# Optimization experiments

Hardware: AMD Instinct MI355X
Metric: run time of the kernel (lower is better)

The kernel has to match this reference:

```python
import jax, jax.numpy as jnp
import numpy as np

N_QUBITS = 10
DEPTH = 5
NUM_CLASSES = 2
DIM = 2 ** N_QUBITS  # 1024


def _rx(t):
    # RX(t) = [[cos(t/2), -i sin(t/2)], [-i sin(t/2), cos(t/2)]]
    c, s = jnp.cos(t / 2), jnp.sin(t / 2)
    zr = jnp.zeros_like(t)
    a = jax.lax.complex(c, zr)
    b = jax.lax.complex(zr, -s)
    return jnp.stack([jnp.stack([a, b]), jnp.stack([b, a])]).astype(jnp.complex64)


def _rz(t):
    # RZ(t) = diag(e^{-it/2}, e^{it/2})
    c, s = jnp.cos(t / 2), jnp.sin(t / 2)
    e = jax.lax.complex(c, -s)
    z = jnp.zeros_like(e)
    return jnp.stack([jnp.stack([e, z]), jnp.stack([z, jnp.conj(e)])]).astype(jnp.complex64)


def _apply_1q(state, U, wire):
    # state: (B, 2, ..., 2); wire axis is wire+1 (wire 0 = most significant bit)
    s = jnp.moveaxis(state, wire + 1, -1)
    s = s @ U.T
    return jnp.moveaxis(s, -1, wire + 1)


def _apply_c1q(state, U, ctrl, tgt):
    # controlled-U: apply U on tgt where ctrl qubit is |1>
    s = jnp.moveaxis(state, ctrl + 1, 1)  # (B, 2_ctrl, rest...)
    ax = tgt + 1 if tgt < ctrl else tgt   # tgt axis inside s[:, k]
    s1 = s[:, 1]
    s1 = jnp.moveaxis(s1, ax, -1) @ U.T
    s1 = jnp.moveaxis(s1, -1, ax)
    s = jnp.stack([s[:, 0], s1], axis=1)
    return jnp.moveaxis(s, 1, ctrl + 1)


def _circuit(x, weights, weights_1, weights_2):
    B = x.shape[0]
    x = x.reshape(B, -1)
    x = jnp.pad(x, ((0, 0), (0, DIM - x.shape[1])))  # pad_with=0
    x = x / jnp.linalg.norm(x, axis=1, keepdims=True)  # normalize=True
    state = jax.lax.complex(x, jnp.zeros_like(x)).reshape((B,) + (2,) * N_QUBITS)
    for d in range(DEPTH):
        for i in range(N_QUBITS):
            state = _apply_1q(state, _rx(weights[d, i, 0]), i)
            state = _apply_1q(state, _rz(weights[d, i, 1]), i)
            state = _apply_1q(state, _rx(weights[d, i, 2]), i)
        r = 1 if d % 2 == 0 else 3  # alternating entangler range (CCQC)
        for i in range(N_QUBITS):
            c = (i + r) % N_QUBITS
            state = _apply_c1q(state, _rz(weights[d, i, 3]), c, i)
            state = _apply_c1q(state, _rx(weights[d, i, 4]), c, i)
        state = _apply_1q(state, _rx(weights_1[d]), 0)
        state = _apply_1q(state, _rz(weights_2[d]), 0)
    probs = (jnp.abs(state) ** 2).reshape(B, DIM)
    # <Z_w> signs: bit w (MSB-first) of each basis index
    bits = (jnp.arange(DIM)[None, :] >> (N_QUBITS - 1 - jnp.arange(N_QUBITS)[:, None])) & 1
    zsign = (1 - 2 * bits).astype(probs.dtype)  # (n_qubits, DIM)
    return probs @ zsign.T  # (B, n_qubits)


def setup_inputs() -> dict:
    key = jax.random.key(0)
    ks = jax.random.split(key, 5)
    B = 8192
    x = jax.random.normal(ks[0], (B, 784), dtype=jnp.float32)
    y = jax.random.randint(ks[1], (B,), 0, NUM_CLASSES)
    weights = jax.random.uniform(ks[2], (DEPTH, N_QUBITS, 5), jnp.float32, 0.0, 2 * np.pi)
    weights_1 = jax.random.uniform(ks[3], (DEPTH,), jnp.float32, 0.0, 2 * np.pi)
    weights_2 = jax.random.uniform(ks[4], (DEPTH,), jnp.float32, 0.0, 2 * np.pi)
    return {"x": x, "y": y, "weights": weights, "weights_1": weights_1, "weights_2": weights_2}


def reference(x, y, weights, weights_1, weights_2):
    expz = _circuit(x, weights, weights_1, weights_2)
    logits = expz[:, :NUM_CLASSES]
    logp = jax.nn.log_softmax(logits, axis=-1)
    nll = -jnp.take_along_axis(logp, y[:, None].astype(jnp.int32), axis=1)[:, 0]
    return jnp.mean(nll)  # CrossEntropyLoss (mean reduction)
```

## Files before the change

kernel.cpp:

```cpp
#include <hip/hip_runtime.h>


namespace {

typedef float f32x2 __attribute__((ext_vector_type(2)));
typedef __fp16 fp16x2 __attribute__((ext_vector_type(2)));
typedef _Float16 f16x8 __attribute__((ext_vector_type(8)));
typedef float f32x4v __attribute__((ext_vector_type(4)));

__device__ __forceinline__ f32x2 pk_mul(f32x2 a, f32x2 b) {
  f32x2 d;
  asm("v_pk_mul_f32 %0, %1, %2" : "=v"(d) : "v"(a), "v"(b));
  return d;
}
__device__ __forceinline__ f32x2 pk_fma(f32x2 a, f32x2 b, f32x2 c) {
  f32x2 d;
  asm("v_pk_fma_f32 %0, %1, %2, %3" : "=v"(d) : "v"(a), "v"(b), "v"(c));
  return d;
}
__device__ __forceinline__ f32x2 pk_fma_swap1(f32x2 a, f32x2 b, f32x2 c) {
  f32x2 d;
  asm("v_pk_fma_f32 %0, %1, %2, %3 op_sel:[0,1,0] op_sel_hi:[1,0,1]"
      : "=v"(d) : "v"(a), "v"(b), "v"(c));
  return d;
}
__device__ __forceinline__ f32x2 cmulp(f32x2 cr2, f32x2 ci2, f32x2 v) {
  return pk_fma_swap1(ci2, v, pk_mul(cr2, v));
}
__device__ __forceinline__ f32x2 cmad(f32x2 acc, f32x2 cr2, f32x2 ci2, f32x2 v) {
  return pk_fma_swap1(ci2, v, pk_fma(cr2, v, acc));
}

__device__ __forceinline__ f32x2 shfl_xor2(f32x2 v, int lm) {
  f32x2 r;
  r.x = __shfl_xor(v.x, lm, 64);
  r.y = __shfl_xor(v.y, lm, 64);
  return r;
}
template <int CTRL>
__device__ __forceinline__ f32x2 dpp_xor2(f32x2 v) {
  f32x2 r;
  const int ix = __builtin_bit_cast(int, v.x);
  const int iy = __builtin_bit_cast(int, v.y);
  r.x = __builtin_bit_cast(float,
      __builtin_amdgcn_update_dpp(0, ix, CTRL, 0xF, 0xF, true));
  r.y = __builtin_bit_cast(float,
      __builtin_amdgcn_update_dpp(0, iy, CTRL, 0xF, 0xF, true));
  return r;
}
__device__ __forceinline__ f32x2 shfl_fast(f32x2 v, const int lm) {
  if (lm == 1) return dpp_xor2<0xB1>(v);
  if (lm == 2) return dpp_xor2<0x4E>(v);
  return shfl_xor2(v, lm);
}
__device__ __forceinline__ f32x2 sel2(bool c, f32x2 a, f32x2 b) {
  f32x2 r; r.x = c ? a.x : b.x; r.y = c ? a.y : b.y; return r;
}

struct c2 { float r, i; };
struct m2c { c2 a00, a01, a10, a11; };

__device__ __forceinline__ c2 cmul(c2 x, c2 y) { return {x.r*y.r - x.i*y.i, x.r*y.i + x.i*y.r}; }
__device__ __forceinline__ c2 cadd(c2 x, c2 y) { return {x.r + y.r, x.i + y.i}; }
__device__ __forceinline__ c2 conjc(c2 a) { return {a.r, -a.i}; }
__device__ __forceinline__ m2c mmul(m2c A, m2c B) {
  m2c C;
  C.a00 = cadd(cmul(A.a00, B.a00), cmul(A.a01, B.a10));
  C.a01 = cadd(cmul(A.a00, B.a01), cmul(A.a01, B.a11));
  C.a10 = cadd(cmul(A.a10, B.a00), cmul(A.a11, B.a10));
  C.a11 = cadd(cmul(A.a10, B.a01), cmul(A.a11, B.a11));
  return C;
}
__device__ __forceinline__ m2c mrx(float t) {
  float c = cosf(0.5f * t), s = sinf(0.5f * t);
  return { {c, 0.f}, {0.f, -s}, {0.f, -s}, {c, 0.f} };
}
__device__ __forceinline__ m2c mrz(float t) {
  float c = cosf(0.5f * t), s = sinf(0.5f * t);
  return { {c, -s}, {0.f, 0.f}, {0.f, 0.f}, {c, s} };
}

__global__ void make_prog(const float* __restrict__ w, const float* __restrict__ w1,
                          const float* __restrict__ w2, float* __restrict__ prog) {
  const int t = threadIdx.x;
  m2c U{}; int slot = -1;
  if (t < 50) {
    const int d = t / 10, i = t % 10;
    const float* p = w + (d * 10 + i) * 5;
    U = mmul(mrx(p[2]), mmul(mrz(p[1]), mrx(p[0])));
    if (i == 0 && d > 0) {
      m2c U0 = mmul(mrz(w2[d - 1]), mrx(w1[d - 1]));
      U = mmul(U, U0);
    }
    const int dd = 4 - d;
    const int base = (dd == 0) ? 0 : 21 + (dd - 1) * 20;
    slot = base + ((d == 4) ? 11 : 10) + (9 - i);
  } else if (t < 100) {
    const int s = t - 50; const int d = s / 10, i = s % 10;
    const float* p = w + (d * 10 + i) * 5;
    U = mmul(mrx(p[4]), mrz(p[3]));
    const int dd = 4 - d;
    const int base = (dd == 0) ? 0 : 21 + (dd - 1) * 20;
    slot = base + ((d == 4) ? 1 : 0) + (9 - i);
  } else if (t == 100) {
    U = mmul(mrz(w2[4]), mrx(w1[4]));
    slot = 0;
  }
  if (slot >= 0) {
    const c2 A[4] = {conjc(U.a00), conjc(U.a10), conjc(U.a01), conjc(U.a11)};
    float* o = prog + slot * 16;
    #pragma unroll
    for (int q = 0; q < 4; ++q) {
      o[q*4 + 0] = A[q].r; o[q*4 + 1] = A[q].r;
      o[q*4 + 2] = -A[q].i; o[q*4 + 3] = A[q].i;
    }
  }
}

struct MatP { f32x2 u00r, u00i, u01r, u01i, u10r, u10i, u11r, u11i; };

__device__ __forceinline__ MatP ldmatG(const float* __restrict__ prog, int slot) {
  const float4* p = reinterpret_cast<const float4*>(prog + slot * 16);
  float4 a = p[0], b = p[1], c = p[2], d = p[3];
  MatP m;
  m.u00r = f32x2{a.x, a.y}; m.u00i = f32x2{a.z, a.w};
  m.u01r = f32x2{b.x, b.y}; m.u01i = f32x2{b.z, b.w};
  m.u10r = f32x2{c.x, c.y}; m.u10i = f32x2{c.z, c.w};
  m.u11r = f32x2{d.x, d.y}; m.u11i = f32x2{d.z, d.w};
  return m;
}

__device__ __forceinline__ void g_xlane(f32x2 (&s)[4], const int lm,
                                        const f32x2 cAr, const f32x2 cAi,
                                        const f32x2 cBr, const f32x2 cBi,
                                        const int cm_reg) {
  #pragma unroll
  for (int k = 0; k < 4; ++k) {
    if (cm_reg && !(k & cm_reg)) continue;
    const f32x2 p = shfl_fast(s[k], lm);
    s[k] = cmad(cmulp(cAr, cAi, s[k]), cBr, cBi, p);
  }
}
__device__ __forceinline__ void g_local(f32x2 (&s)[4], const int kb, const MatP m,
                                        const int cm_reg) {
  const int tm = 1 << kb;
  #pragma unroll
  for (int k0 = 0; k0 < 4; ++k0) {
    if (k0 & tm) continue;
    if (cm_reg && !(k0 & cm_reg)) continue;
    const int k1 = k0 | tm;
    const f32x2 a = s[k0], b = s[k1];
    s[k0] = cmad(cmulp(m.u00r, m.u00i, a), m.u01r, m.u01i, b);
    s[k1] = cmad(cmulp(m.u10r, m.u10i, a), m.u11r, m.u11i, b);
  }
}
__device__ __forceinline__ void g_xwave(f32x2 (&s)[4], f32x2* lxb, const int wv,
                                        const int lane, const int tb,
                                        const f32x2 cAr, const f32x2 cAi,
                                        const f32x2 cBr, const f32x2 cBi,
                                        const int cm_reg) {
  #pragma unroll
  for (int k = 0; k < 4; ++k) lxb[(wv * 4 + k) * 64 + lane] = s[k];
  __syncthreads();
  const int pw = wv ^ (1 << tb);
  #pragma unroll
  for (int k = 0; k < 4; ++k) {
    if (cm_reg && !(k & cm_reg)) continue;
    const f32x2 p = lxb[(pw * 4 + k) * 64 + lane];
    s[k] = cmad(cmulp(cAr, cAi, s[k]), cBr, cBi, p);
  }
}

__device__ __forceinline__ void apply_gate(f32x2 (&s)[4], f32x2* lxb, const int wv,
                                           const int lane, const MatP mIn,
                                           const int bt, const int bc) {
  MatP m = mIn;
  const f32x2 oner{1.f, 1.f}, zero{0.f, 0.f};
  int cm_reg = 0;
  bool fold = false, cl = true;
  if (bc >= 8)      { cl = ((wv >> (bc - 8)) & 1) != 0; fold = true; }
  else if (bc >= 6) { cm_reg = 1 << (bc - 6); }
  else if (bc >= 0) { cl = ((lane >> bc) & 1) != 0; fold = true; }

  if (bt >= 8) {
    const int tb = bt - 8;
    const bool hi = ((wv >> tb) & 1) != 0;
    f32x2 cAr = sel2(hi, m.u11r, m.u00r), cAi = sel2(hi, m.u11i, m.u00i);
    f32x2 cBr = sel2(hi, m.u10r, m.u01r), cBi = sel2(hi, m.u10i, m.u01i);
    if (fold) {
      cAr = sel2(cl, cAr, oner); cAi = sel2(cl, cAi, zero);
      cBr = sel2(cl, cBr, zero); cBi = sel2(cl, cBi, zero);
    }
    g_xwave(s, lxb, wv, lane, tb, cAr, cAi, cBr, cBi, cm_reg);
  } else if (bt >= 6) {
    if (fold) {
      m.u00r = sel2(cl, m.u00r, oner); m.u00i = sel2(cl, m.u00i, zero);
      m.u01r = sel2(cl, m.u01r, zero); m.u01i = sel2(cl, m.u01i, zero);
      m.u10r = sel2(cl, m.u10r, zero); m.u10i = sel2(cl, m.u10i, zero);
      m.u11r = sel2(cl, m.u11r, oner); m.u11i = sel2(cl, m.u11i, zero);
    }
    g_local(s, bt - 6, m, cm_reg);
  } else {
    const bool hi = ((lane >> bt) & 1) != 0;
    f32x2 cAr = sel2(hi, m.u11r, m.u00r), cAi = sel2(hi, m.u11i, m.u00i);
    f32x2 cBr = sel2(hi, m.u10r, m.u01r), cBi = sel2(hi, m.u10i, m.u01i);
    if (fold) {
      cAr = sel2(cl, cAr, oner); cAi = sel2(cl, cAi, zero);
      cBr = sel2(cl, cBr, zero); cBi = sel2(cl, cBi, zero);
    }
    g_xlane(s, 1 << bt, cAr, cAi, cBr, cBi, cm_reg);
  }
}

__global__ __launch_bounds__(256) void qprep(const float* __restrict__ prog,
                                             const float* __restrict__ x,
                                             _Float16* __restrict__ Wt,
                                             _Float16* __restrict__ Xh) {
  const int tid = threadIdx.x;
  if (blockIdx.x >= 1024) {
    const int t = (blockIdx.x - 1024) * 256 + tid;
    const int b = t >> 7;
    const int j = (t & 127) * 8;
    if (j >= 832) return;
    union { fp16x2 h2[4]; f16x8 h8; } u;
    if (j < 784) {
      const float4* p = reinterpret_cast<const float4*>(x + (size_t)b * 784 + j);
      const float4 v0 = p[0], v1 = p[1];
      u.h2[0] = __builtin_amdgcn_cvt_pkrtz(v0.x, v0.y);
      u.h2[1] = __builtin_amdgcn_cvt_pkrtz(v0.z, v0.w);
      u.h2[2] = __builtin_amdgcn_cvt_pkrtz(v1.x, v1.y);
      u.h2[3] = __builtin_amdgcn_cvt_pkrtz(v1.z, v1.w);
    } else {
      #pragma unroll
      for (int q = 0; q < 4; ++q) u.h2[q] = __builtin_amdgcn_cvt_pkrtz(0.f, 0.f);
    }
    *reinterpret_cast<f16x8*>(Xh + (size_t)b * 1024 + j) = u.h8;
    return;
  }

  __shared__ f32x2 lx[2][1024];

  const int lane = tid & 63;
  const int wv = tid >> 6;
  const int n = blockIdx.x;

  f32x2 s[4];
  #pragma unroll
  for (int k = 0; k < 4; ++k) {
    const int j = (wv << 8) | (k << 6) | lane;
    s[k].x = (j == n) ? 1.f : 0.f;
    s[k].y = 0.f;
  }

  int p = 0, ph = 0;
  #pragma unroll
  for (int dd = 0; dd < 5; ++dd) {
    const int d = 4 - dd;
    if (d == 4) {
      apply_gate(s, &lx[ph & 1][0], wv, lane, ldmatG(prog, p), 9, -1);
      ++p; ++ph;
    }
    const int r = (d & 1) ? 3 : 1;
    #pragma unroll
    for (int ii = 0; ii < 10; ++ii) {
      const int i = 9 - ii;
      const int c = (i + r) % 10;
      const int bt = 9 - i, bc = 9 - c;
      apply_gate(s, &lx[ph & 1][0], wv, lane, ldmatG(prog, p), bt, bc);
      ++p; if (bt >= 8) ++ph;
    }
    #pragma unroll
    for (int ii = 0; ii < 10; ++ii) {
      const int i = 9 - ii;
      const int bt = 9 - i;
      apply_gate(s, &lx[ph & 1][0], wv, lane, ldmatG(prog, p), bt, -1);
      ++p; if (bt >= 8) ++ph;
    }
  }

  #pragma unroll
  for (int k = 0; k < 4; ++k) {
    const int j = (wv << 8) | (k << 6) | lane;
    Wt[(size_t)(2 * n) * 1024 + j] = (_Float16)s[k].x;
    Wt[(size_t)(2 * n + 1) * 1024 + j] = (_Float16)(-s[k].y);
  }
}

#define GZ_NSTEP 13

__device__ __forceinline__ void stage_tiles(const _Float16* __restrict__ gA,
                                            const _Float16* __restrict__ gB,
                                            _Float16* sA, _Float16* sB,
                                            int k0, int wv, int lane) {
  const int rIn = lane >> 3;
  const int colh = ((lane & 7) ^ rIn) * 8;
  #pragma unroll
  for (int c = 0; c < 2; ++c) {
    const int chunk = wv * 2 + c;
    const size_t grow = (size_t)(chunk * 8 + rIn) * 1024 + k0 + colh;
    auto* la = (__attribute__((address_space(3))) void*)(sA + chunk * 512 + lane * 8);
    __builtin_amdgcn_global_load_lds(
        (const __attribute__((address_space(1))) void*)(gA + grow), la, 16, 0, 0);
    auto* lb = (__attribute__((address_space(3))) void*)(sB + chunk * 512 + lane * 8);
    __builtin_amdgcn_global_load_lds(
        (const __attribute__((address_space(1))) void*)(gB + grow), lb, 16, 0, 0);
  }
}

__device__ __forceinline__ int lds_off(int row, int slot) {
  return row * 64 + ((slot ^ (row & 7)) * 8);
}

__global__ __launch_bounds__(512) void gemm_z(const _Float16* __restrict__ Xh,
                                              const _Float16* __restrict__ Wt,
                                              float* __restrict__ part, int B) {
  __shared__ _Float16 smA[2][128 * 64];
  __shared__ _Float16 smB[2][128 * 64];

  const int tid = threadIdx.x;
  const int lane = tid & 63;
  const int wv = tid >> 6;
  const int wm = wv >> 1;
  const int wn = wv & 1;
  const int row0 = blockIdx.x * 128;
  const int n0 = blockIdx.y * 128;

  const _Float16* gA = Xh + (size_t)row0 * 1024;
  const _Float16* gB = Wt + (size_t)n0 * 1024;

  const int lr = lane & 15;
  const int lq = lane >> 4;

  f32x4v acc[2][4];
  #pragma unroll
  for (int m = 0; m < 2; ++m)
    #pragma unroll
    for (int f = 0; f < 4; ++f) acc[m][f] = f32x4v{0.f, 0.f, 0.f, 0.f};

  stage_tiles(gA, gB, smA[0], smB[0], 0, wv, lane);
  __syncthreads();

  for (int t = 0; t < GZ_NSTEP; ++t) {
    const int cur = t & 1;
    if (t + 1 < GZ_NSTEP)
      stage_tiles(gA, gB, smA[cur ^ 1], smB[cur ^ 1], (t + 1) * 64, wv, lane);

    #pragma unroll
    for (int kk = 0; kk < 2; ++kk) {
      const int slot = kk * 4 + lq;
      f16x8 a[2], b[4];
      #pragma unroll
      for (int m = 0; m < 2; ++m) {
        const int row = wm * 32 + m * 16 + lr;
        a[m] = *reinterpret_cast<const f16x8*>(&smA[cur][lds_off(row, slot)]);
      }
      #pragma unroll
      for (int f = 0; f < 4; ++f) {
        const int row = wn * 64 + f * 16 + lr;
        b[f] = *reinterpret_cast<const f16x8*>(&smB[cur][lds_off(row, slot)]);
      }
      #pragma unroll
      for (int m = 0; m < 2; ++m)
        #pragma unroll
        for (int f = 0; f < 4; ++f)
          acc[m][f] = __builtin_amdgcn_mfma_f32_16x16x32_f16(a[m], b[f], acc[m][f], 0, 0, 0);
    }
    __syncthreads();
  }

  const int pp = blockIdx.y * 2 + wn;
  #pragma unroll
  for (int m = 0; m < 2; ++m) {
    f32x4v p = f32x4v{0.f, 0.f, 0.f, 0.f};
    #pragma unroll
    for (int f = 0; f < 4; ++f) p += acc[m][f] * acc[m][f];
    #pragma unroll
    for (int msk = 1; msk < 16; msk <<= 1) {
      p.x += __shfl_xor(p.x, msk, 64);
      p.y += __shfl_xor(p.y, msk, 64);
      p.z += __shfl_xor(p.z, msk, 64);
      p.w += __shfl_xor(p.w, msk, 64);
    }
    if (lr == 0) {
      const int rbase = row0 + wm * 32 + m * 16 + lq * 4;
      float* dst = part + (size_t)pp * B + rbase;
      dst[0] = p.x; dst[1] = p.y; dst[2] = p.z; dst[3] = p.w;
    }
  }
}

__global__ __launch_bounds__(256) void nll_part(const float* __restrict__ part,
                                                const int* __restrict__ y,
                                                float* __restrict__ out2, int B) {
  const int row = blockIdx.x * 256 + threadIdx.x;
  float q0 = 0.f, q1 = 0.f, nn = 0.f;
  #pragma unroll
  for (int pp = 0; pp < 32; ++pp) {
    const float P = part[(size_t)pp * B + row];
    q0 += (pp & 16) ? -P : P;
    q1 += (pp & 8) ? -P : P;
    nn += P;
  }
  const float z0 = q0 / nn, z1 = q1 / nn;
  const float mx = fmaxf(z0, z1);
  const float lse = mx + logf(expf(z0 - mx) + expf(z1 - mx));
  const float ly = (y[row] == 0) ? z0 : z1;
  float s = lse - ly;
  #pragma unroll
  for (int msk = 1; msk < 64; msk <<= 1) s += __shfl_xor(s, msk, 64);
  __shared__ float red[4];
  if ((threadIdx.x & 63) == 0) red[threadIdx.x >> 6] = s;
  __syncthreads();
  if (threadIdx.x == 0) out2[blockIdx.x] = red[0] + red[1] + red[2] + red[3];
}

__global__ void nll_final(const float* __restrict__ out2, float* __restrict__ out,
                          int nblk, float scale) {
  const int t = threadIdx.x;
  float s = (t < nblk) ? out2[t] : 0.f;
  #pragma unroll
  for (int msk = 1; msk < 64; msk <<= 1) s += __shfl_xor(s, msk, 64);
  if (t == 0) out[0] = s * scale;
}

}

extern "C" void kernel_launch(void* const* d_in, const int* in_sizes, int n_in,
                              void* d_out, int out_size, void* d_ws, size_t ws_size,
                              hipStream_t stream) {
  const float* x  = (const float*)d_in[0];
  const int*   y  = (const int*)d_in[1];
  const float* w  = (const float*)d_in[2];
  const float* w1 = (const float*)d_in[3];
  const float* w2 = (const float*)d_in[4];
  float* out = (float*)d_out;

  const int B = in_sizes[0] / 784;

  char* ws = (char*)d_ws;
  _Float16* Wt   = (_Float16*)ws;
  _Float16* Xh   = (_Float16*)(ws + (size_t)2048 * 1024 * 2);
  float*    part = (float*)(ws + (size_t)2048 * 1024 * 2 + (size_t)B * 1024 * 2);
  float*    out2 = part + (size_t)32 * B;
  float*    prog = out2 + 64;

  make_prog<<<1, 128, 0, stream>>>(w, w1, w2, prog);
  qprep<<<1024 + (B * 128) / 256, 256, 0, stream>>>(prog, x, Wt, Xh);
  gemm_z<<<dim3(B / 128, 16), 512, 0, stream>>>(Xh, Wt, part, B);
  nll_part<<<B / 256, 256, 0, stream>>>(part, y, out2, B);
  nll_final<<<1, 64, 0, stream>>>(out2, out, B / 256, 1.0f / (float)B);
}
```

Measured before the change: 89.05 us.

## Fuse single-qubit rotation gates into following controlled gates in prep kernel

Folds each single-qubit U1 gate into the next controlled gate on the same target when no intervening gate touches that qubit. The controlled gate then applies V1 on the control=0 branch and VC*V1 on the control=1 branch, which cuts the number of gate passes, shuffles and LDS barriers in the unitary-building qprep kernel. The program layout doubles to two matrices per slot, and the fused path adds select overhead. This affects only the small Wt-generation stage, not the main GEMM.

```diff
diff --git a/kernel.cpp b/kernel.cpp
--- a/kernel.cpp
+++ b/kernel.cpp
@@ -71,6 +71,9 @@
   C.a11 = cadd(cmul(A.a10, B.a01), cmul(A.a11, B.a11));
   return C;
 }
+__device__ __forceinline__ m2c madj(m2c U) {
+  return { conjc(U.a00), conjc(U.a10), conjc(U.a01), conjc(U.a11) };
+}
 __device__ __forceinline__ m2c mrx(float t) {
   float c = cosf(0.5f * t), s = sinf(0.5f * t);
   return { {c, 0.f}, {0.f, -s}, {0.f, -s}, {c, 0.f} };
@@ -80,47 +83,78 @@
   return { {c, -s}, {0.f, 0.f}, {0.f, 0.f}, {c, s} };
 }
 
+__device__ __forceinline__ bool fusable(int d, int i) {
+  return (d & 1) ? (i >= 3) : (i >= 1);
+}
+
 __global__ void make_prog(const float* __restrict__ w, const float* __restrict__ w1,
                           const float* __restrict__ w2, float* __restrict__ prog) {
   const int t = threadIdx.x;
-  m2c U{}; int slot = -1;
-  if (t < 50) {
-    const int d = t / 10, i = t % 10;
-    const float* p = w + (d * 10 + i) * 5;
-    U = mmul(mrx(p[2]), mmul(mrz(p[1]), mrx(p[0])));
+  int kind = -1, od = 0, oi = 0, p = 0;
+  for (int dd = 0; dd < 5; ++dd) {
+    const int d = 4 - dd;
+    if (d == 4) { if (p == t) kind = 0; ++p; }
+    for (int ii = 0; ii < 10; ++ii) {
+      const int i = 9 - ii;
+      if (p == t) { kind = (d <= 3 && fusable(d, i)) ? 2 : 1; od = d; oi = i; }
+      ++p;
+    }
+    for (int ii = 0; ii < 10; ++ii) {
+      const int i = 9 - ii;
+      if (d >= 1 && fusable(d - 1, i)) continue;
+      if (p == t) { kind = 3; od = d; oi = i; }
+      ++p;
+    }
+  }
+  if (kind < 0) return;
+
+  auto u1mat = [&](int d, int i) -> m2c {
+    const float* pw = w + (d * 10 + i) * 5;
+    m2c U = mmul(mrx(pw[2]), mmul(mrz(pw[1]), mrx(pw[0])));
     if (i == 0 && d > 0) {
       m2c U0 = mmul(mrz(w2[d - 1]), mrx(w1[d - 1]));
       U = mmul(U, U0);
     }
-    const int dd = 4 - d;
-    const int base = (dd == 0) ? 0 : 21 + (dd - 1) * 20;
-    slot = base + ((d == 4) ? 11 : 10) + (9 - i);
-  } else if (t < 100) {
-    const int s = t - 50; const int d = s / 10, i = s % 10;
-    const float* p = w + (d * 10 + i) * 5;
-    U = mmul(mrx(p[4]), mrz(p[3]));
-    const int dd = 4 - d;
-    const int base = (dd == 0) ? 0 : 21 + (dd - 1) * 20;
-    slot = base + ((d == 4) ? 1 : 0) + (9 - i);
-  } else if (t == 100) {
-    U = mmul(mrz(w2[4]), mrx(w1[4]));
-    slot = 0;
-  }
-  if (slot >= 0) {
-    const c2 A[4] = {conjc(U.a00), conjc(U.a10), conjc(U.a01), conjc(U.a11)};
-    float* o = prog + slot * 16;
-    #pragma unroll
-    for (int q = 0; q < 4; ++q) {
-      o[q*4 + 0] = A[q].r; o[q*4 + 1] = A[q].r;
-      o[q*4 + 2] = -A[q].i; o[q*4 + 3] = A[q].i;
-    }
+    return U;
+  };
+  auto cumat = [&](int d, int i) -> m2c {
+    const float* pw = w + (d * 10 + i) * 5;
+    return mmul(mrx(pw[4]), mrz(pw[3]));
+  };
+
+  m2c A0{}, A1{};
+  if (kind == 0) {
+    A0 = madj(mmul(mrz(w2[4]), mrx(w1[4])));
+    A1 = A0;
+  } else if (kind == 1) {
+    A0 = madj(cumat(od, oi));
+    A1 = A0;
+  } else if (kind == 2) {
+    m2c V1 = madj(u1mat(od + 1, oi));
+    m2c VC = madj(cumat(od, oi));
+    A0 = V1;
+    A1 = mmul(VC, V1);
+  } else {
+    A0 = madj(u1mat(od, oi));
+    A1 = A0;
+  }
+
+  float* o = prog + t * 32;
+  const c2 e0[4] = {A0.a00, A0.a01, A0.a10, A0.a11};
+  const c2 e1[4] = {A1.a00, A1.a01, A1.a10, A1.a11};
+  #pragma unroll
+  for (int q = 0; q < 4; ++q) {
+    o[q*4 + 0] = e0[q].r; o[q*4 + 1] = e0[q].r;
+    o[q*4 + 2] = -e0[q].i; o[q*4 + 3] = e0[q].i;
+    o[16 + q*4 + 0] = e1[q].r; o[16 + q*4 + 1] = e1[q].r;
+    o[16 + q*4 + 2] = -e1[q].i; o[16 + q*4 + 3] = e1[q].i;
   }
 }
 
 struct MatP { f32x2 u00r, u00i, u01r, u01i, u10r, u10i, u11r, u11i; };
 
-__device__ __forceinline__ MatP ldmatG(const float* __restrict__ prog, int slot) {
-  const float4* p = reinterpret_cast<const float4*>(prog + slot * 16);
+__device__ __forceinline__ MatP ldmatG2(const float* __restrict__ prog, int slot, int half) {
+  const float4* p = reinterpret_cast<const float4*>(prog + slot * 32 + half * 16);
   float4 a = p[0], b = p[1], c = p[2], d = p[3];
   MatP m;
   m.u00r = f32x2{a.x, a.y}; m.u00i = f32x2{a.z, a.w};
@@ -130,44 +164,58 @@
   return m;
 }
 
-__device__ __forceinline__ void g_xlane(f32x2 (&s)[4], const int lm,
-                                        const f32x2 cAr, const f32x2 cAi,
-                                        const f32x2 cBr, const f32x2 cBi,
-                                        const int cm_reg) {
+struct Coef { f32x2 Ar, Ai, Br, Bi; };
+__device__ __forceinline__ Coef mkcoef(const MatP& m, bool hi) {
+  return { sel2(hi, m.u11r, m.u00r), sel2(hi, m.u11i, m.u00i),
+           sel2(hi, m.u10r, m.u01r), sel2(hi, m.u10i, m.u01i) };
+}
+__device__ __forceinline__ Coef coefsel(bool c, const Coef& a, const Coef& b) {
+  return { sel2(c, a.Ar, b.Ar), sel2(c, a.Ai, b.Ai),
+           sel2(c, a.Br, b.Br), sel2(c, a.Bi, b.Bi) };
+}
+__device__ __forceinline__ MatP matsel(bool c, const MatP& a, const MatP& b) {
+  MatP m;
+  m.u00r = sel2(c, a.u00r, b.u00r); m.u00i = sel2(c, a.u00i, b.u00i);
+  m.u01r = sel2(c, a.u01r, b.u01r); m.u01i = sel2(c, a.u01i, b.u01i);
+  m.u10r = sel2(c, a.u10r, b.u10r); m.u10i = sel2(c, a.u10i, b.u10i);
+  m.u11r = sel2(c, a.u11r, b.u11r); m.u11i = sel2(c, a.u11i, b.u11i);
+  return m;
+}
+
+__device__ __forceinline__ void xlane_apply(f32x2 (&s)[4], const int lm,
+                                            const Coef c1, const Coef c0, const int cm) {
   #pragma unroll
   for (int k = 0; k < 4; ++k) {
-    if (cm_reg && !(k & cm_reg)) continue;
+    const Coef& c = (cm && (k & cm)) ? c1 : c0;
     const f32x2 p = shfl_fast(s[k], lm);
-    s[k] = cmad(cmulp(cAr, cAi, s[k]), cBr, cBi, p);
-  }
-}
-__device__ __forceinline__ void g_local(f32x2 (&s)[4], const int kb, const MatP m,
-                                        const int cm_reg) {
+    s[k] = cmad(cmulp(c.Ar, c.Ai, s[k]), c.Br, c.Bi, p);
+  }
+}
+__device__ __forceinline__ void local_apply(f32x2 (&s)[4], const int kb,
+                                            const MatP m1, const MatP m0, const int cm) {
   const int tm = 1 << kb;
   #pragma unroll
   for (int k0 = 0; k0 < 4; ++k0) {
     if (k0 & tm) continue;
-    if (cm_reg && !(k0 & cm_reg)) continue;
     const int k1 = k0 | tm;
+    const MatP& m = (cm && (k0 & cm)) ? m1 : m0;
     const f32x2 a = s[k0], b = s[k1];
     s[k0] = cmad(cmulp(m.u00r, m.u00i, a), m.u01r, m.u01i, b);
     s[k1] = cmad(cmulp(m.u10r, m.u10i, a), m.u11r, m.u11i, b);
   }
 }
-__device__ __forceinline__ void g_xwave(f32x2 (&s)[4], f32x2* lxb, const int wv,
-                                        const int lane, const int tb,
-                                        const f32x2 cAr, const f32x2 cAi,
-                                        const f32x2 cBr, const f32x2 cBi,
-                                        const int cm_reg) {
+__device__ __forceinline__ void xwave_apply(f32x2 (&s)[4], f32x2* lxb, const int wv,
+                                            const int lane, const int tb,
+                                            const Coef c1, const Coef c0, const int cm) {
   #pragma unroll
   for (int k = 0; k < 4; ++k) lxb[(wv * 4 + k) * 64 + lane] = s[k];
   __syncthreads();
   const int pw = wv ^ (1 << tb);
   #pragma unroll
   for (int k = 0; k < 4; ++k) {
-    if (cm_reg && !(k & cm_reg)) continue;
+    const Coef& c = (cm && (k & cm)) ? c1 : c0;
     const f32x2 p = lxb[(pw * 4 + k) * 64 + lane];
-    s[k] = cmad(cmulp(cAr, cAi, s[k]), cBr, cBi, p);
+    s[k] = cmad(cmulp(c.Ar, c.Ai, s[k]), c.Br, c.Bi, p);
   }
 }
 
@@ -185,13 +233,25 @@
   if (bt >= 8) {
     const int tb = bt - 8;
     const bool hi = ((wv >> tb) & 1) != 0;
-    f32x2 cAr = sel2(hi, m.u11r, m.u00r), cAi = sel2(hi, m.u11i, m.u00i);
-    f32x2 cBr = sel2(hi, m.u10r, m.u01r), cBi = sel2(hi, m.u10i, m.u01i);
+    Coef c = mkcoef(m, hi);
     if (fold) {
-      cAr = sel2(cl, cAr, oner); cAi = sel2(cl, cAi, zero);
-      cBr = sel2(cl, cBr, zero); cBi = sel2(cl, cBi, zero);
-    }
-    g_xwave(s, lxb, wv, lane, tb, cAr, cAi, cBr, cBi, cm_reg);
+      c.Ar = sel2(cl, c.Ar, oner); c.Ai = sel2(cl, c.Ai, zero);
+      c.Br = sel2(cl, c.Br, zero); c.Bi = sel2(cl, c.Bi, zero);
+    }
+    if (cm_reg) {
+      #pragma unroll
+      for (int k = 0; k < 4; ++k) lxb[(wv * 4 + k) * 64 + lane] = s[k];
+      __syncthreads();
+      const int pw = wv ^ (1 << tb);
+      #pragma unroll
+      for (int k = 0; k < 4; ++k) {
+        if (!(k & cm_reg)) continue;
+        const f32x2 p = lxb[(pw * 4 + k) * 64 + lane];
+        s[k] = cmad(cmulp(c.Ar, c.Ai, s[k]), c.Br, c.Bi, p);
+      }
+    } else {
+      xwave_apply(s, lxb, wv, lane, tb, c, c, 0);
+    }
   } else if (bt >= 6) {
     if (fold) {
       m.u00r = sel2(cl, m.u00r, oner); m.u00i = sel2(cl, m.u00i, zero);
@@ -199,16 +259,68 @@
       m.u10r = sel2(cl, m.u10r, zero); m.u10i = sel2(cl, m.u10i, zero);
       m.u11r = sel2(cl, m.u11r, oner); m.u11i = sel2(cl, m.u11i, zero);
     }
-    g_local(s, bt - 6, m, cm_reg);
+    const int tm = 1 << (bt - 6);
+    #pragma unroll
+    for (int k0 = 0; k0 < 4; ++k0) {
+      if (k0 & tm) continue;
+      if (cm_reg && !(k0 & cm_reg)) continue;
+      const int k1 = k0 | tm;
+      const f32x2 a = s[k0], b = s[k1];
+      s[k0] = cmad(cmulp(m.u00r, m.u00i, a), m.u01r, m.u01i, b);
+      s[k1] = cmad(cmulp(m.u10r, m.u10i, a), m.u11r, m.u11i, b);
+    }
   } else {
     const bool hi = ((lane >> bt) & 1) != 0;
-    f32x2 cAr = sel2(hi, m.u11r, m.u00r), cAi = sel2(hi, m.u11i, m.u00i);
-    f32x2 cBr = sel2(hi, m.u10r, m.u01r), cBi = sel2(hi, m.u10i, m.u01i);
+    Coef c = mkcoef(m, hi);
     if (fold) {
-      cAr = sel2(cl, cAr, oner); cAi = sel2(cl, cAi, zero);
-      cBr = sel2(cl, cBr, zero); cBi = sel2(cl, cBi, zero);
-    }
-    g_xlane(s, 1 << bt, cAr, cAi, cBr, cBi, cm_reg);
+      c.Ar = sel2(cl, c.Ar, oner); c.Ai = sel2(cl, c.Ai, zero);
+      c.Br = sel2(cl, c.Br, zero); c.Bi = sel2(cl, c.Bi, zero);
+    }
+    const int lm = 1 << bt;
+    #pragma unroll
+    for (int k = 0; k < 4; ++k) {
+      if (cm_reg && !(k & cm_reg)) continue;
+      const f32x2 p = shfl_fast(s[k], lm);
+      s[k] = cmad(cmulp(c.Ar, c.Ai, s[k]), c.Br, c.Bi, p);
+    }
+  }
+}
+
+__device__ __forceinline__ void apply_gate2(f32x2 (&s)[4], f32x2* lxb, const int wv,
+                                            const int lane, const MatP m1, const MatP m0,
+                                            const int bt, const int bc) {
+  int cm = 0; bool cl = true; bool lc = false;
+  if (bc >= 8)      { cl = ((wv >> (bc - 8)) & 1) != 0; lc = true; }
+  else if (bc >= 6) { cm = 1 << (bc - 6); }
+  else              { cl = ((lane >> bc) & 1) != 0; lc = true; }
+
+  if (bt >= 8) {
+    const int tb = bt - 8;
+    const bool hi = ((wv >> tb) & 1) != 0;
+    const Coef c1 = mkcoef(m1, hi), c0 = mkcoef(m0, hi);
+    if (lc) {
+      const Coef cc = coefsel(cl, c1, c0);
+      xwave_apply(s, lxb, wv, lane, tb, cc, cc, 0);
+    } else {
+      xwave_apply(s, lxb, wv, lane, tb, c1, c0, cm);
+    }
+  } else if (bt >= 6) {
+    if (lc) {
+      const MatP m = matsel(cl, m1, m0);
+      local_apply(s, bt - 6, m, m, 0);
+    } else {
+      local_apply(s, bt - 6, m1, m0, cm);
+    }
+  } else {
+    const int lm = 1 << bt;
+    const bool hi = ((lane >> bt) & 1) != 0;
+    const Coef c1 = mkcoef(m1, hi), c0 = mkcoef(m0, hi);
+    if (lc) {
+      const Coef cc = coefsel(cl, c1, c0);
+      xlane_apply(s, lm, cc, cc, 0);
+    } else {
+      xlane_apply(s, lm, c1, c0, cm);
+    }
   }
 }
 
@@ -257,7 +369,7 @@
   for (int dd = 0; dd < 5; ++dd) {
     const int d = 4 - dd;
     if (d == 4) {
-      apply_gate(s, &lx[ph & 1][0], wv, lane, ldmatG(prog, p), 9, -1);
+      apply_gate(s, &lx[ph & 1][0], wv, lane, ldmatG2(prog, p, 0), 9, -1);
       ++p; ++ph;
     }
     const int r = (d & 1) ? 3 : 1;
@@ -266,14 +378,21 @@
       const int i = 9 - ii;
       const int c = (i + r) % 10;
       const int bt = 9 - i, bc = 9 - c;
-      apply_gate(s, &lx[ph & 1][0], wv, lane, ldmatG(prog, p), bt, bc);
+      const bool fused = (d <= 3) && fusable(d, i);
+      if (fused) {
+        apply_gate2(s, &lx[ph & 1][0], wv, lane,
+                    ldmatG2(prog, p, 1), ldmatG2(prog, p, 0), bt, bc);
+      } else {
+        apply_gate(s, &lx[ph & 1][0], wv, lane, ldmatG2(prog, p, 0), bt, bc);
+      }
       ++p; if (bt >= 8) ++ph;
     }
     #pragma unroll
     for (int ii = 0; ii < 10; ++ii) {
       const int i = 9 - ii;
+      if (d >= 1 && fusable(d - 1, i)) continue;
       const int bt = 9 - i;
-      apply_gate(s, &lx[ph & 1][0], wv, lane, ldmatG(prog, p), bt, -1);
+      apply_gate(s, &lx[ph & 1][0], wv, lane, ldmatG2(prog, p, 0), bt, -1);
       ++p; if (bt >= 8) ++ph;
     }
   }
```

Measured after the change: 87.41 us. Within noise of the previous version (-1.8%).
